# Performance work log

Hardware: AMD Instinct MI355X
Metric: run time of the kernel (lower is better)

Reference implementation:

```python
import jax, jax.numpy as jnp
import numpy as np

# AdEx constants (match init_kwargs)
THR = -50.4
EL = -70.6
GL = 30.0
C = 281.0
DELTAT = 2.0
V_RESET = -70.6
TAUW = 144.0
A = 4.0
B = 0.0805
DT = 1.0
N_REFRAC = 5
DAMP = 0.3
DT_GL__C = DT * GL / C
DT_A__TAUW = DT * A / TAUW

BATCH, N_IN, UNITS = 8192, 256, 1024


@jax.custom_vjp
def spike_function(v_scaled):
    return (v_scaled > 0.0).astype(jnp.float32)

def _spike_fwd(v_scaled):
    return spike_function(v_scaled), v_scaled

def _spike_bwd(v_scaled, dy):
    # pseudo-derivative: dampening * max(1 - |v_scaled|, 0)
    return (dy * DAMP * jnp.maximum(1.0 - jnp.abs(v_scaled), 0.0),)

spike_function.defvjp(_spike_fwd, _spike_bwd)


def setup_inputs() -> dict:
    key = jax.random.key(0)
    ks = jax.random.split(key, 7)
    inputs = jax.random.normal(ks[0], (BATCH, N_IN), dtype=jnp.float32)
    old_v = EL + 5.0 * jax.random.normal(ks[1], (BATCH, UNITS), dtype=jnp.float32)
    old_r = jax.random.randint(ks[2], (BATCH, UNITS), 0, N_REFRAC, dtype=jnp.int32)
    old_w = jax.random.normal(ks[3], (BATCH, UNITS), dtype=jnp.float32)
    old_z = (jax.random.uniform(ks[4], (BATCH, UNITS)) < 0.1).astype(jnp.float32)
    input_weights = jax.random.uniform(ks[5], (N_IN, UNITS), dtype=jnp.float32, minval=0.0, maxval=1.2)
    recurrent_weights = 0.7 * jax.random.normal(ks[6], (UNITS, UNITS), dtype=jnp.float32) / np.sqrt(UNITS)
    return {"inputs": inputs, "old_v": old_v, "old_r": old_r, "old_w": old_w,
            "old_z": old_z, "input_weights": input_weights,
            "recurrent_weights": recurrent_weights}


def reference(inputs, old_v, old_r, old_w, old_z, input_weights, recurrent_weights):
    units = recurrent_weights.shape[0]
    disconnect = jnp.eye(units, dtype=bool)  # no autapses on diagonal
    no_autapse_w_rec = jnp.where(disconnect, 0.0, recurrent_weights)

    i_t = inputs @ input_weights + old_z @ no_autapse_w_rec  # (B, U)

    exp_terms = jnp.clip(jnp.exp((old_v - THR) / DELTAT), -1e6, 30.0 / DT_GL__C)
    exp_terms = jax.lax.stop_gradient(exp_terms)

    new_v = (old_v - DT_GL__C * (old_v - EL)
             + DT_GL__C * DELTAT * exp_terms
             + (i_t - old_w) * DT / C)
    new_v = jnp.where(old_z > 0.5, V_RESET, new_v)

    new_w = old_w - DT / TAUW * old_w + DT_A__TAUW * (old_v - EL) + B * old_z

    is_refractory = old_r > 0
    v_scaled = -(THR - new_v) / (THR - EL)
    new_z = spike_function(v_scaled)
    new_z = jnp.where(is_refractory, 0.0, new_z)

    new_r = jnp.clip(old_r - 1 + (new_z * N_REFRAC).astype(jnp.int32), 0, N_REFRAC)

    return new_v, new_z, new_r, new_w
```

## Files before the change

### kernel.cpp

```cpp
#include <hip/hip_runtime.h>
#include <stdint.h>

#define THRC      (-50.4f)
#define ELC       (-70.6f)
#define V_RESETC  (-70.6f)
#define DT_GL_C   (0.10676156583629893f)
#define DELTATC   (2.0f)
#define DT_C      (0.0035587188612099642f)
#define DT_TAUW   (0.006944444444444444f)
#define DTA_TAUW  (0.027777777777777776f)
#define BCONST    (0.0805f)
#define EXPCLIP   (281.0f)

#define M_TOT 8192
#define UNITS 1024
#define K_TOT 1792
#define CH    (8192*1024)
#define BM 128
#define BN 64
#define NKSTEPS (K_TOT/32)

typedef __attribute__((ext_vector_type(8))) short s16x8;
typedef __attribute__((ext_vector_type(4))) float f32x4;

__device__ __forceinline__ unsigned short f2bf(float f) {
  union { float f; unsigned int u; } v; v.f = f;
  unsigned int r = v.u + 0x7fffu + ((v.u >> 16) & 1u);
  return (unsigned short)(r >> 16);
}
__device__ __forceinline__ float bf2f(unsigned short h) {
  union { unsigned int u; float f; } v; v.u = ((unsigned int)h) << 16; return v.f;
}

__device__ __forceinline__ void gload_lds16(const void* g, void* l) {
  __builtin_amdgcn_global_load_lds(
      (const __attribute__((address_space(1))) void*)g,
      (__attribute__((address_space(3))) void*)l, 16, 0, 0);
}

__device__ __forceinline__ int swz_col(int row, int k) {
  return (k & ~31) | (((((k >> 3) & 3) ^ ((row >> 1) & 3)) << 3)) | (k & 7);
}

__global__ __launch_bounds__(256) void build_a(const float* __restrict__ X,
                                               const float* __restrict__ Z,
                                               unsigned short* __restrict__ A) {
  int o = blockIdx.x * 256 + threadIdx.x;
  int row = o / 224;
  int c8 = (o - row * 224) * 8;
  const float* src; bool lo = false;
  if (c8 < 256)        { src = X + (size_t)row * 256 + c8; }
  else if (c8 < 512)   { src = X + (size_t)row * 256 + (c8 - 256); lo = true; }
  else if (c8 < 768)   { src = X + (size_t)row * 256 + (c8 - 512); }
  else                 { src = Z + (size_t)row * 1024 + (c8 - 768); }
  float4 f0 = *(const float4*)(src);
  float4 f1 = *(const float4*)(src + 4);
  float fv[8] = {f0.x, f0.y, f0.z, f0.w, f1.x, f1.y, f1.z, f1.w};
  unsigned short h[8];
#pragma unroll
  for (int i = 0; i < 8; ++i) {
    unsigned short hi = f2bf(fv[i]);
    h[i] = lo ? f2bf(fv[i] - bf2f(hi)) : hi;
  }
  uint4 pk;
  pk.x = (unsigned)h[0] | ((unsigned)h[1] << 16);
  pk.y = (unsigned)h[2] | ((unsigned)h[3] << 16);
  pk.z = (unsigned)h[4] | ((unsigned)h[5] << 16);
  pk.w = (unsigned)h[6] | ((unsigned)h[7] << 16);
  *(uint4*)(A + (size_t)row * K_TOT + swz_col(row, c8)) = pk;
}

__global__ __launch_bounds__(256) void build_b(const float* __restrict__ Wi,
                                               const float* __restrict__ Wr,
                                               unsigned short* __restrict__ BT) {
  __shared__ unsigned short tile[32][33];
  int tx = threadIdx.x & 31, ty = threadIdx.x >> 5;
  int k0 = blockIdx.x * 32, n0 = blockIdx.y * 32;
#pragma unroll
  for (int j = 0; j < 4; ++j) {
    int kk = k0 + ty + j * 8;
    int n  = n0 + tx;
    float f; bool lo = false;
    if (kk < 256)       f = Wi[(size_t)kk * 1024 + n];
    else if (kk < 512)  f = Wi[(size_t)(kk - 256) * 1024 + n];
    else if (kk < 768) { f = Wi[(size_t)(kk - 512) * 1024 + n]; lo = true; }
    else { int kr = kk - 768; f = (kr == n) ? 0.0f : Wr[(size_t)kr * 1024 + n]; }
    unsigned short h = f2bf(f);
    if (lo) h = f2bf(f - bf2f(h));
    tile[ty + j * 8][tx] = h;
  }
  __syncthreads();
#pragma unroll
  for (int j = 0; j < 4; ++j) {
    int n  = n0 + ty + j * 8;
    int kk = k0 + tx;
    BT[(size_t)n * K_TOT + swz_col(n, kk)] = tile[tx][ty + j * 8];
  }
}

__global__ __launch_bounds__(256, 4) void adex_gemm(
    const unsigned short* __restrict__ A, const unsigned short* __restrict__ BT,
    const float* __restrict__ oV, const int* __restrict__ oR,
    const float* __restrict__ oW, const float* __restrict__ oZ,
    float* __restrict__ out)
{
  __shared__ unsigned short As[2][BM * 32];
  __shared__ unsigned short Bs[2][BN * 32];
  const int tid  = threadIdx.x;
  const int wid  = tid >> 6;
  const int lane = tid & 63;
  const int mt = blockIdx.x & 63;
  const int nt = blockIdx.x >> 6;
  const int rowA0 = mt * BM;
  const int colB0 = nt * BN;

  f32x4 acc[4][2];
#pragma unroll
  for (int i = 0; i < 4; ++i)
#pragma unroll
    for (int j = 0; j < 2; ++j) acc[i][j] = (f32x4){0.f, 0.f, 0.f, 0.f};

  const int srow = tid >> 2, sslot = tid & 3;
  const unsigned short* aS0 = A  + (size_t)(rowA0 + srow) * K_TOT + sslot * 8;
  const unsigned short* aS1 = aS0 + (size_t)64 * K_TOT;
  const unsigned short* bS  = BT + (size_t)(colB0 + srow) * K_TOT + sslot * 8;

  const int l15 = lane & 15, l4 = lane >> 4;
  const int wr = (wid >> 1) * 64, wc = (wid & 1) * 32;
  const int slot = l4 ^ ((l15 >> 1) & 3);
  int offA[4], offB[2];
#pragma unroll
  for (int f = 0; f < 4; ++f) offA[f] = (wr + f * 16 + l15) * 32 + slot * 8;
#pragma unroll
  for (int f = 0; f < 2; ++f) offB[f] = (wc + f * 16 + l15) * 32 + slot * 8;

#define STAGE(buf)                                            \
  do {                                                        \
    gload_lds16(aS0, &As[buf][0] + tid * 8);                  \
    gload_lds16(aS1, &As[buf][0] + 2048 + tid * 8);           \
    gload_lds16(bS,  &Bs[buf][0] + tid * 8);                  \
    aS0 += 32; aS1 += 32; bS += 32;                           \
  } while (0)

  STAGE(0);
  asm volatile("s_waitcnt vmcnt(0)" ::: "memory");
  __syncthreads();

  int cur = 0;
  for (int ks = 0; ks < NKSTEPS; ++ks) {
    if (ks + 1 < NKSTEPS) STAGE(cur ^ 1);
    const unsigned short* ab = &As[cur][0];
    const unsigned short* bb = &Bs[cur][0];
    s16x8 af[4], bfv[2];
#pragma unroll
    for (int f = 0; f < 4; ++f) af[f]  = *(const s16x8*)(ab + offA[f]);
#pragma unroll
    for (int f = 0; f < 2; ++f) bfv[f] = *(const s16x8*)(bb + offB[f]);
#pragma unroll
    for (int i = 0; i < 4; ++i)
#pragma unroll
      for (int j = 0; j < 2; ++j)
        acc[i][j] = __builtin_amdgcn_mfma_f32_16x16x32_bf16(af[i], bfv[j], acc[i][j], 0, 0, 0);
    asm volatile("s_waitcnt vmcnt(0)" ::: "memory");
    __syncthreads();
    cur ^= 1;
  }
#undef STAGE

#pragma unroll
  for (int i = 0; i < 4; ++i) {
    int mBase = rowA0 + wr + i * 16 + l4 * 4;
#pragma unroll
    for (int j = 0; j < 2; ++j) {
      int u = colB0 + wc + j * 16 + l15;
#pragma unroll
      for (int r = 0; r < 4; ++r) {
        int m = mBase + r;
        size_t idx = (size_t)m * UNITS + u;
        float it = acc[i][j][r];
        float ov = oV[idx];
        float ow = oW[idx];
        float oz = oZ[idx];
        int   orr = oR[idx];
        float ex = expf((ov - THRC) * 0.5f);
        ex = fminf(ex, EXPCLIP);
        float nv = ov - DT_GL_C * (ov - ELC) + (DT_GL_C * DELTATC) * ex + (it - ow) * DT_C;
        nv = (oz > 0.5f) ? V_RESETC : nv;
        float nw = ow - DT_TAUW * ow + DTA_TAUW * (ov - ELC) + BCONST * oz;
        float nz = (nv > THRC) ? 1.0f : 0.0f;
        if (orr > 0) nz = 0.0f;
        int nr = orr - 1 + (nz > 0.5f ? 5 : 0);
        nr = nr < 0 ? 0 : (nr > 5 ? 5 : nr);
        out[idx]           = nv;
        out[CH + idx]      = nz;
        out[2 * CH + idx]  = (float)nr;
        out[3 * CH + idx]  = nw;
      }
    }
  }
}

extern "C" void kernel_launch(void* const* d_in, const int* in_sizes, int n_in,
                              void* d_out, int out_size, void* d_ws, size_t ws_size,
                              hipStream_t stream) {
  const float* X  = (const float*)d_in[0];
  const float* oV = (const float*)d_in[1];
  const int*   oR = (const int*)d_in[2];
  const float* oW = (const float*)d_in[3];
  const float* oZ = (const float*)d_in[4];
  const float* Wi = (const float*)d_in[5];
  const float* Wr = (const float*)d_in[6];
  unsigned short* Aall = (unsigned short*)d_ws;
  unsigned short* BT   = Aall + (size_t)M_TOT * K_TOT;
  float* out = (float*)d_out;

  hipLaunchKernelGGL(build_a, dim3((M_TOT * (K_TOT / 8)) / 256), dim3(256), 0, stream, X, oZ, Aall);
  hipLaunchKernelGGL(build_b, dim3(K_TOT / 32, UNITS / 32), dim3(256), 0, stream, Wi, Wr, BT);
  hipLaunchKernelGGL(adex_gemm, dim3((M_TOT / BM) * (UNITS / BN)), dim3(256), 0, stream,
                     Aall, BT, oV, oR, oW, oZ, out);
}
```

Baseline: 146.9 us.

## Triple-buffer LDS staging with partial vmcnt waits and swizzle block order

Replaces the double-buffered LDS pipeline with three buffers, so global-to-LDS loads run two k-steps ahead. Each step waits only on the older loads (vmcnt(3)) before a single barrier, instead of draining everything. Block IDs are also remapped so that neighbouring blocks share A and B tiles, which should improve L2 reuse. LDS use per block grows by half, which may lower occupancy, and correctness now depends on the vmcnt counting matching the three loads issued per stage.

```diff
diff --git a/kernel.cpp b/kernel.cpp
--- a/kernel.cpp
+++ b/kernel.cpp
@@ -19,6 +19,8 @@
 #define BM 128
 #define BN 64
 #define NKSTEPS (K_TOT/32)
+#define NBUF 3
+#define BUFE ((BM + BN) * 32)
 
 typedef __attribute__((ext_vector_type(8))) short s16x8;
 typedef __attribute__((ext_vector_type(4))) float f32x4;
@@ -104,13 +106,15 @@
     const float* __restrict__ oW, const float* __restrict__ oZ,
     float* __restrict__ out)
 {
-  __shared__ unsigned short As[2][BM * 32];
-  __shared__ unsigned short Bs[2][BN * 32];
+  __shared__ unsigned short S[NBUF][BUFE];
   const int tid  = threadIdx.x;
   const int wid  = tid >> 6;
   const int lane = tid & 63;
-  const int mt = blockIdx.x & 63;
-  const int nt = blockIdx.x >> 6;
+
+  const int bid = blockIdx.x;
+  const int swz = (bid & 7) * 128 + (bid >> 3);
+  const int nt = swz & 15;
+  const int mt = swz >> 4;
   const int rowA0 = mt * BM;
   const int colB0 = nt * BN;
 
@@ -132,38 +136,40 @@
 #pragma unroll
   for (int f = 0; f < 4; ++f) offA[f] = (wr + f * 16 + l15) * 32 + slot * 8;
 #pragma unroll
-  for (int f = 0; f < 2; ++f) offB[f] = (wc + f * 16 + l15) * 32 + slot * 8;
+  for (int f = 0; f < 2; ++f) offB[f] = (BM * 32) + (wc + f * 16 + l15) * 32 + slot * 8;
 
 #define STAGE(buf)                                            \
   do {                                                        \
-    gload_lds16(aS0, &As[buf][0] + tid * 8);                  \
-    gload_lds16(aS1, &As[buf][0] + 2048 + tid * 8);           \
-    gload_lds16(bS,  &Bs[buf][0] + tid * 8);                  \
+    gload_lds16(aS0, &S[buf][0] + tid * 8);                   \
+    gload_lds16(aS1, &S[buf][0] + 2048 + tid * 8);            \
+    gload_lds16(bS,  &S[buf][0] + 4096 + tid * 8);            \
     aS0 += 32; aS1 += 32; bS += 32;                           \
   } while (0)
 
   STAGE(0);
-  asm volatile("s_waitcnt vmcnt(0)" ::: "memory");
-  __syncthreads();
-
-  int cur = 0;
+  STAGE(1);
+
+  int kb = 0;
   for (int ks = 0; ks < NKSTEPS; ++ks) {
-    if (ks + 1 < NKSTEPS) STAGE(cur ^ 1);
-    const unsigned short* ab = &As[cur][0];
-    const unsigned short* bb = &Bs[cur][0];
+    if (ks + 1 < NKSTEPS) asm volatile("s_waitcnt vmcnt(3)" ::: "memory");
+    else                  asm volatile("s_waitcnt vmcnt(0)" ::: "memory");
+    __builtin_amdgcn_s_barrier();
+    if (ks + 2 < NKSTEPS) {
+      int nb = kb + 2; if (nb >= NBUF) nb -= NBUF;
+      STAGE(nb);
+    }
+    const unsigned short* base = &S[kb][0];
     s16x8 af[4], bfv[2];
 #pragma unroll
-    for (int f = 0; f < 4; ++f) af[f]  = *(const s16x8*)(ab + offA[f]);
-#pragma unroll
-    for (int f = 0; f < 2; ++f) bfv[f] = *(const s16x8*)(bb + offB[f]);
+    for (int f = 0; f < 4; ++f) af[f]  = *(const s16x8*)(base + offA[f]);
+#pragma unroll
+    for (int f = 0; f < 2; ++f) bfv[f] = *(const s16x8*)(base + offB[f]);
 #pragma unroll
     for (int i = 0; i < 4; ++i)
 #pragma unroll
       for (int j = 0; j < 2; ++j)
         acc[i][j] = __builtin_amdgcn_mfma_f32_16x16x32_bf16(af[i], bfv[j], acc[i][j], 0, 0, 0);
-    asm volatile("s_waitcnt vmcnt(0)" ::: "memory");
-    __syncthreads();
-    cur ^= 1;
+    ++kb; if (kb >= NBUF) kb -= NBUF;
   }
 #undef STAGE
 
```

After: 151.4 us. +3.0%, slower.

## Pack spike matrix as bitmask and expand to bf16 in registers; enlarge GEMM tile

Applied to the files above, without the earlier changes.

The binary old_z matrix is no longer stored as bf16 inside the A operand. A new kernel packs it into a bitmask via ballot, and the GEMM expands the bits to bf16 ones and zeros in registers for the recurrent K range. This cuts A-operand global traffic for that range by about 16x and removes the fp32 oZ read in the epilogue. The block tile also grows to 256x128 with 512 threads, which raises B reuse but adds VALU work for bit expansion and lowers occupancy.

```diff
diff --git a/kernel.cpp b/kernel.cpp
--- a/kernel.cpp
+++ b/kernel.cpp
@@ -14,11 +14,12 @@
 
 #define M_TOT 8192
 #define UNITS 1024
-#define K_TOT 1792
+#define KX    768
+#define KBT   1792
 #define CH    (8192*1024)
-#define BM 128
-#define BN 64
-#define NKSTEPS (K_TOT/32)
+#define BM 256
+#define BN 128
+#define ZSLAB (M_TOT*16)
 
 typedef __attribute__((ext_vector_type(8))) short s16x8;
 typedef __attribute__((ext_vector_type(4))) float f32x4;
@@ -31,28 +32,24 @@
 __device__ __forceinline__ float bf2f(unsigned short h) {
   union { unsigned int u; float f; } v; v.u = ((unsigned int)h) << 16; return v.f;
 }
-
 __device__ __forceinline__ void gload_lds16(const void* g, void* l) {
   __builtin_amdgcn_global_load_lds(
       (const __attribute__((address_space(1))) void*)g,
       (__attribute__((address_space(3))) void*)l, 16, 0, 0);
 }
-
 __device__ __forceinline__ int swz_col(int row, int k) {
   return (k & ~31) | (((((k >> 3) & 3) ^ ((row >> 1) & 3)) << 3)) | (k & 7);
 }
 
-__global__ __launch_bounds__(256) void build_a(const float* __restrict__ X,
-                                               const float* __restrict__ Z,
-                                               unsigned short* __restrict__ A) {
+__global__ __launch_bounds__(256) void build_ax(const float* __restrict__ X,
+                                                unsigned short* __restrict__ AX) {
   int o = blockIdx.x * 256 + threadIdx.x;
-  int row = o / 224;
-  int c8 = (o - row * 224) * 8;
+  int row = o / 96;
+  int c8 = (o - row * 96) * 8;
   const float* src; bool lo = false;
   if (c8 < 256)        { src = X + (size_t)row * 256 + c8; }
   else if (c8 < 512)   { src = X + (size_t)row * 256 + (c8 - 256); lo = true; }
-  else if (c8 < 768)   { src = X + (size_t)row * 256 + (c8 - 512); }
-  else                 { src = Z + (size_t)row * 1024 + (c8 - 768); }
+  else                 { src = X + (size_t)row * 256 + (c8 - 512); }
   float4 f0 = *(const float4*)(src);
   float4 f1 = *(const float4*)(src + 4);
   float fv[8] = {f0.x, f0.y, f0.z, f0.w, f1.x, f1.y, f1.z, f1.w};
@@ -67,7 +64,7 @@
   pk.y = (unsigned)h[2] | ((unsigned)h[3] << 16);
   pk.z = (unsigned)h[4] | ((unsigned)h[5] << 16);
   pk.w = (unsigned)h[6] | ((unsigned)h[7] << 16);
-  *(uint4*)(A + (size_t)row * K_TOT + swz_col(row, c8)) = pk;
+  *(uint4*)(AX + (size_t)row * KX + swz_col(row, c8)) = pk;
 }
 
 __global__ __launch_bounds__(256) void build_b(const float* __restrict__ Wi,
@@ -94,93 +91,166 @@
   for (int j = 0; j < 4; ++j) {
     int n  = n0 + ty + j * 8;
     int kk = k0 + tx;
-    BT[(size_t)n * K_TOT + swz_col(n, kk)] = tile[tx][ty + j * 8];
-  }
-}
-
-__global__ __launch_bounds__(256, 4) void adex_gemm(
-    const unsigned short* __restrict__ A, const unsigned short* __restrict__ BT,
+    BT[(size_t)n * KBT + swz_col(n, kk)] = tile[tx][ty + j * 8];
+  }
+}
+
+__global__ __launch_bounds__(256) void build_zb(const float* __restrict__ Z,
+                                                char* __restrict__ Zb) {
+  int ge = blockIdx.x * 256 + threadIdx.x;
+  float val = Z[ge];
+  unsigned long long mask = __ballot(val > 0.5f);
+  if ((threadIdx.x & 63) == 0) {
+    int row = ge >> 10;
+    int k0  = ge & 1023;
+    *(unsigned long long*)(Zb + (size_t)(k0 >> 7) * ZSLAB + row * 16 + ((k0 >> 3) & 15)) = mask;
+  }
+}
+
+__device__ __forceinline__ s16x8 expand_bits(unsigned zw, int l4) {
+  unsigned b = zw >> (l4 * 8);
+  s16x8 a;
+#pragma unroll
+  for (int e = 0; e < 8; ++e)
+    a[e] = (short)(((b >> e) & 1u) ? 0x3F80 : 0);
+  return a;
+}
+
+__global__ __launch_bounds__(512, 2) void adex_gemm(
+    const unsigned short* __restrict__ AX, const unsigned short* __restrict__ BT,
+    const char* __restrict__ Zb,
     const float* __restrict__ oV, const int* __restrict__ oR,
-    const float* __restrict__ oW, const float* __restrict__ oZ,
-    float* __restrict__ out)
+    const float* __restrict__ oW, float* __restrict__ out)
 {
-  __shared__ unsigned short As[2][BM * 32];
-  __shared__ unsigned short Bs[2][BN * 32];
+  __shared__ unsigned short S[2][12288];
   const int tid  = threadIdx.x;
-  const int wid  = tid >> 6;
+  const int w    = tid >> 6;
   const int lane = tid & 63;
-  const int mt = blockIdx.x & 63;
-  const int nt = blockIdx.x >> 6;
+  const int l15  = lane & 15, l4 = lane >> 4;
+  const int wm   = w >> 1, wn = w & 1;
+
+  const int bid = blockIdx.x;
+  const int mt = bid >> 3, nt = bid & 7;
   const int rowA0 = mt * BM;
   const int colB0 = nt * BN;
 
-  f32x4 acc[4][2];
+  const int srow = tid >> 2, sslot = tid & 3;
+  const unsigned short* aS0 = AX + (size_t)(rowA0 + srow)       * KX  + sslot * 8;
+  const unsigned short* aS1 = AX + (size_t)(rowA0 + 128 + srow) * KX  + sslot * 8;
+  const unsigned short* bS  = BT + (size_t)(colB0 + srow)       * KBT + sslot * 8;
+
+#define STAGE_A(buf)                                          \
+  do { gload_lds16(aS0, &S[buf][0] + tid * 8);                \
+       gload_lds16(aS1, &S[buf][0] + 4096 + tid * 8); } while (0)
+#define STAGE_B(buf) gload_lds16(bS, &S[buf][0] + 8192 + tid * 8)
+
+  const int slot = l4 ^ ((l15 >> 1) & 3);
+  int offA[4], offB[4];
+#pragma unroll
+  for (int f = 0; f < 4; ++f) offA[f] = (wm * 64 + f * 16 + l15) * 32 + slot * 8;
+#pragma unroll
+  for (int f = 0; f < 4; ++f) offB[f] = 8192 + (wn * 64 + f * 16 + l15) * 32 + slot * 8;
+
+  const char* zp0 = Zb + (size_t)(rowA0 + wm * 64 +  0 + l15) * 16;
+  const char* zp1 = Zb + (size_t)(rowA0 + wm * 64 + 16 + l15) * 16;
+  const char* zp2 = Zb + (size_t)(rowA0 + wm * 64 + 32 + l15) * 16;
+  const char* zp3 = Zb + (size_t)(rowA0 + wm * 64 + 48 + l15) * 16;
+
+  f32x4 acc[4][4];
 #pragma unroll
   for (int i = 0; i < 4; ++i)
 #pragma unroll
-    for (int j = 0; j < 2; ++j) acc[i][j] = (f32x4){0.f, 0.f, 0.f, 0.f};
-
-  const int srow = tid >> 2, sslot = tid & 3;
-  const unsigned short* aS0 = A  + (size_t)(rowA0 + srow) * K_TOT + sslot * 8;
-  const unsigned short* aS1 = aS0 + (size_t)64 * K_TOT;
-  const unsigned short* bS  = BT + (size_t)(colB0 + srow) * K_TOT + sslot * 8;
-
-  const int l15 = lane & 15, l4 = lane >> 4;
-  const int wr = (wid >> 1) * 64, wc = (wid & 1) * 32;
-  const int slot = l4 ^ ((l15 >> 1) & 3);
-  int offA[4], offB[2];
-#pragma unroll
-  for (int f = 0; f < 4; ++f) offA[f] = (wr + f * 16 + l15) * 32 + slot * 8;
-#pragma unroll
-  for (int f = 0; f < 2; ++f) offB[f] = (wc + f * 16 + l15) * 32 + slot * 8;
-
-#define STAGE(buf)                                            \
-  do {                                                        \
-    gload_lds16(aS0, &As[buf][0] + tid * 8);                  \
-    gload_lds16(aS1, &As[buf][0] + 2048 + tid * 8);           \
-    gload_lds16(bS,  &Bs[buf][0] + tid * 8);                  \
-    aS0 += 32; aS1 += 32; bS += 32;                           \
-  } while (0)
-
-  STAGE(0);
+    for (int j = 0; j < 4; ++j) acc[i][j] = (f32x4){0.f, 0.f, 0.f, 0.f};
+
+  STAGE_A(0); STAGE_B(0);
+  uint4 zbE0 = *(const uint4*)zp0, zbE1 = *(const uint4*)zp1;
+  uint4 zbE2 = *(const uint4*)zp2, zbE3 = *(const uint4*)zp3;
   asm volatile("s_waitcnt vmcnt(0)" ::: "memory");
   __syncthreads();
 
   int cur = 0;
-  for (int ks = 0; ks < NKSTEPS; ++ks) {
-    if (ks + 1 < NKSTEPS) STAGE(cur ^ 1);
-    const unsigned short* ab = &As[cur][0];
-    const unsigned short* bb = &Bs[cur][0];
-    s16x8 af[4], bfv[2];
-#pragma unroll
-    for (int f = 0; f < 4; ++f) af[f]  = *(const s16x8*)(ab + offA[f]);
-#pragma unroll
-    for (int f = 0; f < 2; ++f) bfv[f] = *(const s16x8*)(bb + offB[f]);
+#pragma unroll 2
+  for (int ks = 0; ks < 24; ++ks) {
+    if (ks < 23) { aS0 += 32; aS1 += 32; bS += 32; STAGE_A(cur ^ 1); STAGE_B(cur ^ 1); }
+    else         { bS += 32; STAGE_B(cur ^ 1); }
+    const unsigned short* base = &S[cur][0];
+    s16x8 af[4], bf[4];
+#pragma unroll
+    for (int f = 0; f < 4; ++f) af[f] = *(const s16x8*)(base + offA[f]);
+#pragma unroll
+    for (int f = 0; f < 4; ++f) bf[f] = *(const s16x8*)(base + offB[f]);
 #pragma unroll
     for (int i = 0; i < 4; ++i)
 #pragma unroll
-      for (int j = 0; j < 2; ++j)
-        acc[i][j] = __builtin_amdgcn_mfma_f32_16x16x32_bf16(af[i], bfv[j], acc[i][j], 0, 0, 0);
+      for (int j = 0; j < 4; ++j)
+        acc[i][j] = __builtin_amdgcn_mfma_f32_16x16x32_bf16(af[i], bf[j], acc[i][j], 0, 0, 0);
     asm volatile("s_waitcnt vmcnt(0)" ::: "memory");
     __syncthreads();
     cur ^= 1;
   }
-#undef STAGE
-
+
+#define ZSTEP(W0, W1, W2, W3, DOSTAGE)                                        \
+  do {                                                                        \
+    if (DOSTAGE) { bS += 32; STAGE_B(cur ^ 1); }                              \
+    const unsigned short* base = &S[cur][0];                                  \
+    s16x8 az[4];                                                              \
+    az[0] = expand_bits(W0, l4); az[1] = expand_bits(W1, l4);                 \
+    az[2] = expand_bits(W2, l4); az[3] = expand_bits(W3, l4);                 \
+    s16x8 bf[4];                                                              \
+    bf[0] = *(const s16x8*)(base + offB[0]);                                  \
+    bf[1] = *(const s16x8*)(base + offB[1]);                                  \
+    bf[2] = *(const s16x8*)(base + offB[2]);                                  \
+    bf[3] = *(const s16x8*)(base + offB[3]);                                  \
+    _Pragma("unroll")                                                         \
+    for (int i = 0; i < 4; ++i)                                               \
+      _Pragma("unroll")                                                       \
+      for (int j = 0; j < 4; ++j)                                             \
+        acc[i][j] = __builtin_amdgcn_mfma_f32_16x16x32_bf16(az[i], bf[j], acc[i][j], 0, 0, 0); \
+    asm volatile("s_waitcnt vmcnt(0)" ::: "memory");                          \
+    __syncthreads();                                                          \
+    cur ^= 1;                                                                 \
+  } while (0)
+
+  uint4 zbO0, zbO1, zbO2, zbO3;
+  for (int gp = 0; gp < 4; ++gp) {
+    zp0 += ZSLAB; zp1 += ZSLAB; zp2 += ZSLAB; zp3 += ZSLAB;
+    zbO0 = *(const uint4*)zp0; zbO1 = *(const uint4*)zp1;
+    zbO2 = *(const uint4*)zp2; zbO3 = *(const uint4*)zp3;
+    ZSTEP(zbE0.x, zbE1.x, zbE2.x, zbE3.x, true);
+    ZSTEP(zbE0.y, zbE1.y, zbE2.y, zbE3.y, true);
+    ZSTEP(zbE0.z, zbE1.z, zbE2.z, zbE3.z, true);
+    ZSTEP(zbE0.w, zbE1.w, zbE2.w, zbE3.w, true);
+    if (gp < 3) {
+      zp0 += ZSLAB; zp1 += ZSLAB; zp2 += ZSLAB; zp3 += ZSLAB;
+      zbE0 = *(const uint4*)zp0; zbE1 = *(const uint4*)zp1;
+      zbE2 = *(const uint4*)zp2; zbE3 = *(const uint4*)zp3;
+    }
+    ZSTEP(zbO0.x, zbO1.x, zbO2.x, zbO3.x, true);
+    ZSTEP(zbO0.y, zbO1.y, zbO2.y, zbO3.y, true);
+    ZSTEP(zbO0.z, zbO1.z, zbO2.z, zbO3.z, true);
+    ZSTEP(zbO0.w, zbO1.w, zbO2.w, zbO3.w, gp < 3);
+  }
+#undef ZSTEP
+#undef STAGE_A
+#undef STAGE_B
+
+  const char* zslab = Zb + (size_t)nt * ZSLAB;
 #pragma unroll
   for (int i = 0; i < 4; ++i) {
-    int mBase = rowA0 + wr + i * 16 + l4 * 4;
-#pragma unroll
-    for (int j = 0; j < 2; ++j) {
-      int u = colB0 + wc + j * 16 + l15;
-#pragma unroll
-      for (int r = 0; r < 4; ++r) {
-        int m = mBase + r;
+#pragma unroll
+    for (int r = 0; r < 4; ++r) {
+      int m = rowA0 + wm * 64 + i * 16 + l4 * 4 + r;
+      unsigned zwA = *(const unsigned*)(zslab + m * 16 + (wn * 2 + 0) * 4);
+      unsigned zwB = *(const unsigned*)(zslab + m * 16 + (wn * 2 + 1) * 4);
+#pragma unroll
+      for (int j = 0; j < 4; ++j) {
+        int u = colB0 + wn * 64 + j * 16 + l15;
         size_t idx = (size_t)m * UNITS + u;
         float it = acc[i][j][r];
+        unsigned zw = (j < 2) ? zwA : zwB;
+        float oz = ((zw >> ((j & 1) * 16 + l15)) & 1u) ? 1.0f : 0.0f;
         float ov = oV[idx];
         float ow = oW[idx];
-        float oz = oZ[idx];
         int   orr = oR[idx];
         float ex = expf((ov - THRC) * 0.5f);
         ex = fminf(ex, EXPCLIP);
@@ -210,12 +280,14 @@
   const float* oZ = (const float*)d_in[4];
   const float* Wi = (const float*)d_in[5];
   const float* Wr = (const float*)d_in[6];
-  unsigned short* Aall = (unsigned short*)d_ws;
-  unsigned short* BT   = Aall + (size_t)M_TOT * K_TOT;
+  unsigned short* AX = (unsigned short*)d_ws;
+  unsigned short* BT = AX + (size_t)M_TOT * KX;
+  char*           Zb = (char*)(BT + (size_t)UNITS * KBT);
   float* out = (float*)d_out;
 
-  hipLaunchKernelGGL(build_a, dim3((M_TOT * (K_TOT / 8)) / 256), dim3(256), 0, stream, X, oZ, Aall);
-  hipLaunchKernelGGL(build_b, dim3(K_TOT / 32, UNITS / 32), dim3(256), 0, stream, Wi, Wr, BT);
-  hipLaunchKernelGGL(adex_gemm, dim3((M_TOT / BM) * (UNITS / BN)), dim3(256), 0, stream,
-                     Aall, BT, oV, oR, oW, oZ, out);
-}
+  hipLaunchKernelGGL(build_ax, dim3((M_TOT * (KX / 8)) / 256), dim3(256), 0, stream, X, AX);
+  hipLaunchKernelGGL(build_b,  dim3(KBT / 32, UNITS / 32), dim3(256), 0, stream, Wi, Wr, BT);
+  hipLaunchKernelGGL(build_zb, dim3((M_TOT * UNITS) / 256), dim3(256), 0, stream, oZ, Zb);
+  hipLaunchKernelGGL(adex_gemm, dim3((M_TOT / BM) * (UNITS / BN)), dim3(512), 0, stream,
+                     AX, BT, Zb, oV, oR, oW, out);
+}
```

Result: faster. 133.9 us (-8.9%).
